# Kernel optimization log

Hardware: AMD Instinct MI355X
Metric: run time of the kernel (lower is better)

The kernel has to match this reference:

```python
import jax, jax.numpy as jnp
import numpy as np

IN_FEATURES = 4096
OUT_FEATURES = 4096  # % 16 == 0, so pad_out = 0
BATCH, SEQ = 4, 2048


def setup_inputs() -> dict:
    key = jax.random.key(0)
    k_x, k_w, k_b = jax.random.split(key, 3)
    # int8 activations and weights (W8A8)
    x = jax.random.randint(k_x, (BATCH, SEQ, IN_FEATURES), -128, 128, dtype=jnp.int32).astype(jnp.int8)
    # weight stored as (in_features, out_features), matching qlinear.weight layout
    weight = jax.random.randint(k_w, (IN_FEATURES, OUT_FEATURES), -128, 128, dtype=jnp.int32).astype(jnp.int8)
    # a: scalar input scale; b: per-output-channel dequant/requant scale
    a = jnp.full((1, 1), 0.0123, dtype=jnp.float32)
    b = jax.random.uniform(k_b, (1, OUT_FEATURES), dtype=jnp.float32, minval=0.001, maxval=0.02)
    return {"x": x, "weight": weight, "a": a, "b": b}


def reference(x, weight, a, b):
    # x: [B, S, K] int8; weight: [K, N] int8; a: [1,1] f32; b: [1,N] f32
    x_shape = x.shape
    x2d = x.reshape(-1, x_shape[-1])
    acc = jnp.matmul(x2d, weight, preferred_element_type=jnp.int32)
    # fused dequant (scalar a) + per-channel requant (b), round-to-nearest, saturate to int8
    y_f = acc.astype(jnp.float32) * a * b  # [T, N]
    y = jnp.clip(jnp.round(y_f), -128.0, 127.0).astype(jnp.int8)
    return y.reshape(*x_shape[:-1], -1)
```

## Files before the change

kernel.cpp:

```cpp
#include <hip/hip_runtime.h>
#include <stdint.h>

#define M_DIM 8192
#define N_DIM 4096
#define K_DIM 4096
#define BM 128
#define BN 128
#define BK 64

typedef int v4i __attribute__((ext_vector_type(4)));
typedef unsigned u32;

__device__ __forceinline__ void gll16(const void* g, void* l) {
  __builtin_amdgcn_global_load_lds(
      (const __attribute__((address_space(1))) void*)g,
      (__attribute__((address_space(3))) void*)l, 16, 0, 0);
}

__device__ __forceinline__ u32 pack4(const int4 v) {
  return (v.x & 0xffu) | ((v.y & 0xffu) << 8) | ((v.z & 0xffu) << 16) |
         ((u32)(v.w & 0xffu) << 24);
}

__global__ __launch_bounds__(256) void detect_i32(const int* __restrict__ X,
                                                  u32* __restrict__ flag) {
  __shared__ int ok;
  if (threadIdx.x == 0) ok = 1;
  __syncthreads();
  int good = 1;
  for (int i = threadIdx.x; i < 1024; i += 256) {
    const int w = X[i];
    good &= (w == (int)(int8_t)(w & 0xff));
  }
  if (!good) atomicAnd(&ok, 0);
  __syncthreads();
  if (threadIdx.x == 0) *flag = (u32)ok;
}

__global__ __launch_bounds__(256) void pack_x_ad(const void* __restrict__ Xin,
                                                 u32* __restrict__ out,
                                                 const u32* __restrict__ flag) {
  const bool i32 = (*flag != 0);
  const int base = blockIdx.x * 1024 + threadIdx.x;
  if (i32) {
    const int4* in = (const int4*)Xin;
#pragma unroll
    for (int j = 0; j < 4; ++j) {
      const int idx = base + j * 256;
      out[idx] = pack4(in[idx]);
    }
  } else {
    const u32* in = (const u32*)Xin;
#pragma unroll
    for (int j = 0; j < 4; ++j) {
      const int idx = base + j * 256;
      out[idx] = in[idx];
    }
  }
}

__global__ __launch_bounds__(256) void packT_w_ad(const void* __restrict__ Wv,
                                                  int8_t* __restrict__ WT,
                                                  const u32* __restrict__ flag) {
  __shared__ u32 lds[64 * 21];
  const bool i32 = (*flag != 0);
  const int tid = threadIdx.x;
  const int tk = blockIdx.x & 63;
  const int tn = blockIdx.x >> 6;
  const int k0 = tk * 64, n0 = tn * 64;

#pragma unroll
  for (int j = 0; j < 4; ++j) {
    const int id = j * 256 + tid;
    const int k = id >> 4, c = id & 15;
    u32 word;
    if (i32) {
      const int4 v =
          *(const int4*)((const int*)Wv + (size_t)(k0 + k) * N_DIM + n0 + c * 4);
      word = pack4(v);
    } else {
      word = *(const u32*)((const int8_t*)Wv + (size_t)(k0 + k) * N_DIM + n0 +
                           c * 4);
    }
    lds[k * 21 + c] = word;
  }
  __syncthreads();
  const int kd = tid & 15, nq = tid >> 4;
  const u32 d0 = lds[(kd * 4 + 0) * 21 + nq];
  const u32 d1 = lds[(kd * 4 + 1) * 21 + nq];
  const u32 d2 = lds[(kd * 4 + 2) * 21 + nq];
  const u32 d3 = lds[(kd * 4 + 3) * 21 + nq];
  u32* outp = (u32*)WT;
#pragma unroll
  for (int i = 0; i < 4; ++i) {
    const u32 e = ((d0 >> (8 * i)) & 0xffu) | (((d1 >> (8 * i)) & 0xffu) << 8) |
                  (((d2 >> (8 * i)) & 0xffu) << 16) |
                  (((d3 >> (8 * i)) & 0xffu) << 24);
    const int n = n0 + nq * 4 + i;
    outp[(size_t)n * (K_DIM / 4) + (k0 / 4) + kd] = e;
  }
}

__device__ __forceinline__ void epilogue(const v4i acc[4][4], float a,
                                         const float* __restrict__ bScale,
                                         int* __restrict__ Y, int bm, int bn,
                                         int wm, int wn, int quad, int l16) {
  const int nBase = bn * BN + wn * 64 + l16;
  float bs[4];
#pragma unroll
  for (int ni = 0; ni < 4; ++ni) bs[ni] = bScale[nBase + ni * 16];
#pragma unroll
  for (int mi = 0; mi < 4; ++mi) {
    const int m0 = bm * BM + wm * 64 + mi * 16 + quad * 4;
#pragma unroll
    for (int r = 0; r < 4; ++r) {
      int* row = Y + (size_t)(m0 + r) * N_DIM + nBase;
#pragma unroll
      for (int ni = 0; ni < 4; ++ni) {
        float v = ((float)acc[mi][ni][r] * a) * bs[ni];
        v = rintf(v);
        v = fminf(fmaxf(v, -128.f), 127.f);
        row[ni * 16] = (int)v;
      }
    }
  }
}

__global__ __launch_bounds__(512, 2) void gemm_256(
    const int8_t* __restrict__ X, const int8_t* __restrict__ WT,
    const float* __restrict__ aScale, const float* __restrict__ bScale,
    int* __restrict__ Y) {
  __shared__ __align__(16) int8_t lds[131072];
  const int tid = threadIdx.x;
  const int lane = tid & 63;
  const int wave = tid >> 6;
  const int quad = lane >> 4, l16 = lane & 15;
  const int wm = wave >> 2, wn = wave & 3;

  const int swz = (blockIdx.x & 7) * 64 + (blockIdx.x >> 3);
  const int bn = swz & 15, bm = swz >> 4;

  const int clog = (((tid & 3) ^ ((tid >> 3) & 3)) << 4);
  const int pc = quad ^ ((l16 >> 1) & 3);

  const int8_t* xa = X + (size_t)(bm * 256 + (tid >> 2)) * K_DIM + clog;
  const int8_t* xb = WT + (size_t)(bn * 256 + (tid >> 2)) * K_DIM + clog;
  int8_t* ldsA = lds + tid * 16;
  int8_t* ldsB = lds + 65536 + tid * 16;
  const int8_t* aBase = lds + (wm * 128 + l16) * 64 + pc * 16;
  const int8_t* bBase = lds + 65536 + (wn * 64 + l16) * 64 + pc * 16;

  v4i acc[8][4] = {};

  gll16(xa, ldsA);
  gll16(xa + (size_t)128 * K_DIM, ldsA + 8192);
  gll16(xb, ldsB);
  gll16(xb + (size_t)128 * K_DIM, ldsB + 8192);
  gll16(xa + 64, ldsA + 16384);
  gll16(xa + (size_t)128 * K_DIM + 64, ldsA + 16384 + 8192);
  gll16(xb + 64, ldsB + 16384);
  gll16(xb + (size_t)128 * K_DIM + 64, ldsB + 16384 + 8192);
  asm volatile("s_waitcnt vmcnt(4)" ::: "memory");
  __builtin_amdgcn_s_barrier();

  for (int g = 0; g < 64; ++g) {
    const int soff = (g & 3) << 14;
    const int poff = ((g + 2) & 3) << 14;
    const bool pre = (g + 2) < 64;
    v4i af[4], bf[4];
#pragma unroll
    for (int i = 0; i < 4; ++i)
      af[i] = *(const v4i*)(aBase + soff + i * 1024);
#pragma unroll
    for (int i = 0; i < 4; ++i)
      bf[i] = *(const v4i*)(bBase + soff + i * 1024);
    if (pre) {
      const int8_t* s = xa + (size_t)(g + 2) * 64;
      gll16(s, ldsA + poff);
      gll16(s + (size_t)128 * K_DIM, ldsA + poff + 8192);
    }
    __builtin_amdgcn_s_barrier();
    asm volatile("s_waitcnt lgkmcnt(0)" ::: "memory");
    __builtin_amdgcn_sched_barrier(0);
    __builtin_amdgcn_s_setprio(1);
#pragma unroll
    for (int mi = 0; mi < 4; ++mi)
#pragma unroll
      for (int ni = 0; ni < 4; ++ni)
        acc[mi][ni] = __builtin_amdgcn_mfma_i32_16x16x64_i8(
            af[mi], bf[ni], acc[mi][ni], 0, 0, 0);
    __builtin_amdgcn_s_setprio(0);
    __builtin_amdgcn_s_barrier();

#pragma unroll
    for (int i = 0; i < 4; ++i)
      af[i] = *(const v4i*)(aBase + soff + 4096 + i * 1024);
    if (pre) {
      const int8_t* s = xb + (size_t)(g + 2) * 64;
      gll16(s, ldsB + poff);
      gll16(s + (size_t)128 * K_DIM, ldsB + poff + 8192);
    }
    __builtin_amdgcn_s_barrier();
    asm volatile("s_waitcnt lgkmcnt(0)" ::: "memory");
    __builtin_amdgcn_sched_barrier(0);
    __builtin_amdgcn_s_setprio(1);
#pragma unroll
    for (int mi = 0; mi < 4; ++mi)
#pragma unroll
      for (int ni = 0; ni < 4; ++ni)
        acc[4 + mi][ni] = __builtin_amdgcn_mfma_i32_16x16x64_i8(
            af[mi], bf[ni], acc[4 + mi][ni], 0, 0, 0);
    __builtin_amdgcn_s_setprio(0);
    if (g <= 61)
      asm volatile("s_waitcnt vmcnt(4)" ::: "memory");
    else
      asm volatile("s_waitcnt vmcnt(0)" ::: "memory");
    __builtin_amdgcn_s_barrier();
  }

  const float a = aScale[0];
  const int nBase = bn * 256 + wn * 64 + l16;
  float bs[4];
#pragma unroll
  for (int ni = 0; ni < 4; ++ni) bs[ni] = bScale[nBase + ni * 16];
#pragma unroll
  for (int mi = 0; mi < 8; ++mi) {
    const int m0 = bm * 256 + wm * 128 + mi * 16 + quad * 4;
#pragma unroll
    for (int r = 0; r < 4; ++r) {
      int* row = Y + (size_t)(m0 + r) * N_DIM + nBase;
#pragma unroll
      for (int ni = 0; ni < 4; ++ni) {
        float v = ((float)acc[mi][ni][r] * a) * bs[ni];
        v = rintf(v);
        v = fminf(fmaxf(v, -128.f), 127.f);
        row[ni * 16] = (int)v;
      }
    }
  }
}

__global__ __launch_bounds__(256) void gemm_inA(
    const void* __restrict__ Xv, const int8_t* __restrict__ WT,
    const float* __restrict__ aScale, const float* __restrict__ bScale,
    int* __restrict__ Y, const u32* __restrict__ flag) {
  __shared__ __align__(16) int8_t As[BM * BK];
  __shared__ __align__(16) int8_t Bs[BN * BK];
  const bool i32 = (*flag != 0);
  const int tid = threadIdx.x;
  const int lane = tid & 63, wave = tid >> 6;
  const int quad = lane >> 4, l16 = lane & 15;
  const int wm = wave & 1, wn = wave >> 1;
  const int bn = blockIdx.x & 31;
  const int bm = blockIdx.x >> 5;

  const int r0 = tid >> 2;
  const int c0 = (tid & 3) * 16;
  const int8_t* Bg0 = WT + (size_t)(bn * BN + r0) * K_DIM + c0;
  const int8_t* Bg1 = Bg0 + (size_t)64 * K_DIM;
  int8_t* Al0 = As + tid * 16;
  int8_t* Al1 = Al0 + 4096;
  int8_t* Bl0 = Bs + tid * 16;
  int8_t* Bl1 = Bl0 + 4096;

  v4i acc[4][4] = {};
  const int8_t* aLds = As + (wm * 64 + l16) * BK + quad * 16;
  const int8_t* bLds = Bs + (wn * 64 + l16) * BK + quad * 16;

  if (i32) {
    const int* Xg0 = (const int*)Xv + (size_t)(bm * BM + r0) * K_DIM + c0;
    const int* Xg1 = Xg0 + (size_t)64 * K_DIM;
    for (int k0 = 0; k0 < K_DIM; k0 += BK) {
      gll16(Bg0 + k0, Bl0);
      gll16(Bg1 + k0, Bl1);
      const int4* p0 = (const int4*)(Xg0 + k0);
      const int4* p1 = (const int4*)(Xg1 + k0);
      uint4 w0, w1;
      w0.x = pack4(p0[0]); w0.y = pack4(p0[1]);
      w0.z = pack4(p0[2]); w0.w = pack4(p0[3]);
      w1.x = pack4(p1[0]); w1.y = pack4(p1[1]);
      w1.z = pack4(p1[2]); w1.w = pack4(p1[3]);
      *(uint4*)Al0 = w0;
      *(uint4*)Al1 = w1;
      __syncthreads();
      v4i af[4], bf[4];
#pragma unroll
      for (int i = 0; i < 4; ++i) af[i] = *(const v4i*)(aLds + i * 16 * BK);
#pragma unroll
      for (int i = 0; i < 4; ++i) bf[i] = *(const v4i*)(bLds + i * 16 * BK);
#pragma unroll
      for (int mi = 0; mi < 4; ++mi)
#pragma unroll
        for (int ni = 0; ni < 4; ++ni)
          acc[mi][ni] = __builtin_amdgcn_mfma_i32_16x16x64_i8(
              af[mi], bf[ni], acc[mi][ni], 0, 0, 0);
      __syncthreads();
    }
  } else {
    const int8_t* Ag0 = (const int8_t*)Xv + (size_t)(bm * BM + r0) * K_DIM + c0;
    const int8_t* Ag1 = Ag0 + (size_t)64 * K_DIM;
    for (int k0 = 0; k0 < K_DIM; k0 += BK) {
      gll16(Ag0 + k0, Al0);
      gll16(Ag1 + k0, Al1);
      gll16(Bg0 + k0, Bl0);
      gll16(Bg1 + k0, Bl1);
      __syncthreads();
      v4i af[4], bf[4];
#pragma unroll
      for (int i = 0; i < 4; ++i) af[i] = *(const v4i*)(aLds + i * 16 * BK);
#pragma unroll
      for (int i = 0; i < 4; ++i) bf[i] = *(const v4i*)(bLds + i * 16 * BK);
#pragma unroll
      for (int mi = 0; mi < 4; ++mi)
#pragma unroll
        for (int ni = 0; ni < 4; ++ni)
          acc[mi][ni] = __builtin_amdgcn_mfma_i32_16x16x64_i8(
              af[mi], bf[ni], acc[mi][ni], 0, 0, 0);
      __syncthreads();
    }
  }
  epilogue(acc, aScale[0], bScale, Y, bm, bn, wm, wn, quad, l16);
}

extern "C" void kernel_launch(void* const* d_in, const int* in_sizes, int n_in,
                              void* d_out, int out_size, void* d_ws,
                              size_t ws_size, hipStream_t stream) {
  const void* Xv = d_in[0];
  const void* Wv = d_in[1];
  const float* a = (const float*)d_in[2];
  const float* b = (const float*)d_in[3];
  int* Y = (int*)d_out;

  const size_t xB = (size_t)M_DIM * K_DIM;
  const size_t wB = (size_t)N_DIM * K_DIM;

  if (ws_size >= xB + wB + 64) {
    int8_t* Xp = (int8_t*)d_ws;
    int8_t* WT = (int8_t*)d_ws + xB;
    u32* flag = (u32*)((int8_t*)d_ws + xB + wB);
    detect_i32<<<1, 256, 0, stream>>>((const int*)Xv, flag);
    pack_x_ad<<<(M_DIM * K_DIM / 4) / 1024, 256, 0, stream>>>(Xv, (u32*)Xp,
                                                              flag);
    packT_w_ad<<<(K_DIM / 64) * (N_DIM / 64), 256, 0, stream>>>(Wv, WT, flag);
    gemm_256<<<(M_DIM / 256) * (N_DIM / 256), 512, 0, stream>>>(Xp, WT, a, b,
                                                                Y);
  } else if (ws_size >= wB + 64) {
    int8_t* WT = (int8_t*)d_ws;
    u32* flag = (u32*)((int8_t*)d_ws + wB);
    detect_i32<<<1, 256, 0, stream>>>((const int*)Xv, flag);
    packT_w_ad<<<(K_DIM / 64) * (N_DIM / 64), 256, 0, stream>>>(Wv, WT, flag);
    gemm_inA<<<(M_DIM / BM) * (N_DIM / BN), 256, 0, stream>>>(Xv, WT, a, b, Y,
                                                              flag);
  } else {
    int8_t* WT = (int8_t*)d_ws;
    u32* flag = (u32*)((int8_t*)d_ws + (ws_size >= wB + 4 ? wB : 0));
    detect_i32<<<1, 256, 0, stream>>>((const int*)Xv, flag);
    packT_w_ad<<<(K_DIM / 64) * (N_DIM / 64), 256, 0, stream>>>(Wv, WT, flag);
    gemm_inA<<<(M_DIM / BM) * (N_DIM / BN), 256, 0, stream>>>(Xv, WT, a, b, Y,
                                                              flag);
  }
}
```

Baseline: 408.0 us.

## Switch GEMM to 32x32x32 int8 MFMA, deepen prefetch, inline dtype detection

The main 256x256 GEMM now uses 32x32x32 int8 MFMA tiles with v16i accumulators instead of 16x16x64 tiles. This halves the B-fragment register count per wave, and the epilogue is rewritten for the 32x32 output layout. The global-to-LDS prefetch goes from two stages ahead to three stages ahead, using all four LDS slots, with the vmcnt waits adjusted to match. The separate detect_i32 kernel launch is dropped on the main path: each pack block now re-checks the input header itself, which trades a launch and a dependency for redundant small reads per block.

```diff
diff --git a/kernel.cpp b/kernel.cpp
--- a/kernel.cpp
+++ b/kernel.cpp
@@ -9,6 +9,7 @@
 #define BK 64
 
 typedef int v4i __attribute__((ext_vector_type(4)));
+typedef int v16i __attribute__((ext_vector_type(16)));
 typedef unsigned u32;
 
 __device__ __forceinline__ void gll16(const void* g, void* l) {
@@ -22,25 +23,31 @@
          ((u32)(v.w & 0xffu) << 24);
 }
 
+__device__ __forceinline__ bool hdr_is_i32(const int* __restrict__ X, int tid,
+                                           int* ok) {
+  if (tid == 0) *ok = 1;
+  __syncthreads();
+  int good = 1;
+  for (int i = tid; i < 1024; i += 256) {
+    const int w = X[i];
+    good &= (w == (int)(int8_t)(w & 0xff));
+  }
+  if (!good) atomicAnd(ok, 0);
+  __syncthreads();
+  return *ok != 0;
+}
+
 __global__ __launch_bounds__(256) void detect_i32(const int* __restrict__ X,
                                                   u32* __restrict__ flag) {
   __shared__ int ok;
-  if (threadIdx.x == 0) ok = 1;
-  __syncthreads();
-  int good = 1;
-  for (int i = threadIdx.x; i < 1024; i += 256) {
-    const int w = X[i];
-    good &= (w == (int)(int8_t)(w & 0xff));
-  }
-  if (!good) atomicAnd(&ok, 0);
-  __syncthreads();
-  if (threadIdx.x == 0) *flag = (u32)ok;
-}
-
-__global__ __launch_bounds__(256) void pack_x_ad(const void* __restrict__ Xin,
-                                                 u32* __restrict__ out,
-                                                 const u32* __restrict__ flag) {
-  const bool i32 = (*flag != 0);
+  const bool i32 = hdr_is_i32(X, threadIdx.x, &ok);
+  if (threadIdx.x == 0) *flag = i32 ? 1u : 0u;
+}
+
+__global__ __launch_bounds__(256) void pack_x_f(const void* __restrict__ Xin,
+                                                u32* __restrict__ out) {
+  __shared__ int ok;
+  const bool i32 = hdr_is_i32((const int*)Xin, threadIdx.x, &ok);
   const int base = blockIdx.x * 1024 + threadIdx.x;
   if (i32) {
     const int4* in = (const int4*)Xin;
@@ -59,12 +66,13 @@
   }
 }
 
-__global__ __launch_bounds__(256) void packT_w_ad(const void* __restrict__ Wv,
-                                                  int8_t* __restrict__ WT,
-                                                  const u32* __restrict__ flag) {
+__global__ __launch_bounds__(256) void packT_w_f(const void* __restrict__ Wv,
+                                                 int8_t* __restrict__ WT,
+                                                 const int* __restrict__ Xhdr) {
   __shared__ u32 lds[64 * 21];
-  const bool i32 = (*flag != 0);
+  __shared__ int ok;
   const int tid = threadIdx.x;
+  const bool i32 = hdr_is_i32(Xhdr, tid, &ok);
   const int tk = blockIdx.x & 63;
   const int tn = blockIdx.x >> 6;
   const int k0 = tk * 64, n0 = tn * 64;
@@ -134,48 +142,51 @@
   const int tid = threadIdx.x;
   const int lane = tid & 63;
   const int wave = tid >> 6;
-  const int quad = lane >> 4, l16 = lane & 15;
+  const int l31 = lane & 31, h = lane >> 5;
   const int wm = wave >> 2, wn = wave & 3;
 
-  const int swz = (blockIdx.x & 7) * 64 + (blockIdx.x >> 3);
-  const int bn = swz & 15, bm = swz >> 4;
+  const int swzb = (blockIdx.x & 7) * 64 + (blockIdx.x >> 3);
+  const int bn = swzb & 15, bm = swzb >> 4;
 
   const int clog = (((tid & 3) ^ ((tid >> 3) & 3)) << 4);
-  const int pc = quad ^ ((l16 >> 1) & 3);
+  const int sw = (l31 >> 1) & 3;
+  const int pc0 = (h ^ sw) << 4;
+  const int pc1 = pc0 ^ 32;
 
   const int8_t* xa = X + (size_t)(bm * 256 + (tid >> 2)) * K_DIM + clog;
   const int8_t* xb = WT + (size_t)(bn * 256 + (tid >> 2)) * K_DIM + clog;
   int8_t* ldsA = lds + tid * 16;
   int8_t* ldsB = lds + 65536 + tid * 16;
-  const int8_t* aBase = lds + (wm * 128 + l16) * 64 + pc * 16;
-  const int8_t* bBase = lds + 65536 + (wn * 64 + l16) * 64 + pc * 16;
-
-  v4i acc[8][4] = {};
-
-  gll16(xa, ldsA);
-  gll16(xa + (size_t)128 * K_DIM, ldsA + 8192);
-  gll16(xb, ldsB);
-  gll16(xb + (size_t)128 * K_DIM, ldsB + 8192);
-  gll16(xa + 64, ldsA + 16384);
-  gll16(xa + (size_t)128 * K_DIM + 64, ldsA + 16384 + 8192);
-  gll16(xb + 64, ldsB + 16384);
-  gll16(xb + (size_t)128 * K_DIM + 64, ldsB + 16384 + 8192);
-  asm volatile("s_waitcnt vmcnt(4)" ::: "memory");
+  const int8_t* aB0 = lds + (wm * 128 + l31) * 64 + pc0;
+  const int8_t* aB1 = lds + (wm * 128 + l31) * 64 + pc1;
+  const int8_t* bB0 = lds + 65536 + (wn * 64 + l31) * 64 + pc0;
+  const int8_t* bB1 = lds + 65536 + (wn * 64 + l31) * 64 + pc1;
+
+  v16i acc[4][2] = {};
+
+#pragma unroll
+  for (int t = 0; t < 3; ++t) {
+    gll16(xa + t * 64, ldsA + t * 16384);
+    gll16(xa + (size_t)128 * K_DIM + t * 64, ldsA + t * 16384 + 8192);
+    gll16(xb + t * 64, ldsB + t * 16384);
+    gll16(xb + (size_t)128 * K_DIM + t * 64, ldsB + t * 16384 + 8192);
+  }
+  asm volatile("s_waitcnt vmcnt(8)" ::: "memory");
   __builtin_amdgcn_s_barrier();
 
   for (int g = 0; g < 64; ++g) {
     const int soff = (g & 3) << 14;
-    const int poff = ((g + 2) & 3) << 14;
-    const bool pre = (g + 2) < 64;
-    v4i af[4], bf[4];
-#pragma unroll
-    for (int i = 0; i < 4; ++i)
-      af[i] = *(const v4i*)(aBase + soff + i * 1024);
-#pragma unroll
-    for (int i = 0; i < 4; ++i)
-      bf[i] = *(const v4i*)(bBase + soff + i * 1024);
+    const int poff = ((g + 3) & 3) << 14;
+    const bool pre = g <= 60;
+    v4i af[4], bf[2];
+#pragma unroll
+    for (int mi = 0; mi < 4; ++mi)
+      af[mi] = *(const v4i*)(aB0 + soff + mi * 2048);
+#pragma unroll
+    for (int ni = 0; ni < 2; ++ni)
+      bf[ni] = *(const v4i*)(bB0 + soff + ni * 2048);
     if (pre) {
-      const int8_t* s = xa + (size_t)(g + 2) * 64;
+      const int8_t* s = xa + (size_t)(g + 3) * 64;
       gll16(s, ldsA + poff);
       gll16(s + (size_t)128 * K_DIM, ldsA + poff + 8192);
     }
@@ -186,17 +197,20 @@
 #pragma unroll
     for (int mi = 0; mi < 4; ++mi)
 #pragma unroll
-      for (int ni = 0; ni < 4; ++ni)
-        acc[mi][ni] = __builtin_amdgcn_mfma_i32_16x16x64_i8(
+      for (int ni = 0; ni < 2; ++ni)
+        acc[mi][ni] = __builtin_amdgcn_mfma_i32_32x32x32_i8(
             af[mi], bf[ni], acc[mi][ni], 0, 0, 0);
     __builtin_amdgcn_s_setprio(0);
     __builtin_amdgcn_s_barrier();
 
 #pragma unroll
-    for (int i = 0; i < 4; ++i)
-      af[i] = *(const v4i*)(aBase + soff + 4096 + i * 1024);
+    for (int mi = 0; mi < 4; ++mi)
+      af[mi] = *(const v4i*)(aB1 + soff + mi * 2048);
+#pragma unroll
+    for (int ni = 0; ni < 2; ++ni)
+      bf[ni] = *(const v4i*)(bB1 + soff + ni * 2048);
     if (pre) {
-      const int8_t* s = xb + (size_t)(g + 2) * 64;
+      const int8_t* s = xb + (size_t)(g + 3) * 64;
       gll16(s, ldsB + poff);
       gll16(s + (size_t)128 * K_DIM, ldsB + poff + 8192);
     }
@@ -207,11 +221,13 @@
 #pragma unroll
     for (int mi = 0; mi < 4; ++mi)
 #pragma unroll
-      for (int ni = 0; ni < 4; ++ni)
-        acc[4 + mi][ni] = __builtin_amdgcn_mfma_i32_16x16x64_i8(
-            af[mi], bf[ni], acc[4 + mi][ni], 0, 0, 0);
+      for (int ni = 0; ni < 2; ++ni)
+        acc[mi][ni] = __builtin_amdgcn_mfma_i32_32x32x32_i8(
+            af[mi], bf[ni], acc[mi][ni], 0, 0, 0);
     __builtin_amdgcn_s_setprio(0);
-    if (g <= 61)
+    if (g < 61)
+      asm volatile("s_waitcnt vmcnt(8)" ::: "memory");
+    else if (g == 61)
       asm volatile("s_waitcnt vmcnt(4)" ::: "memory");
     else
       asm volatile("s_waitcnt vmcnt(0)" ::: "memory");
@@ -219,22 +235,23 @@
   }
 
   const float a = aScale[0];
-  const int nBase = bn * 256 + wn * 64 + l16;
-  float bs[4];
-#pragma unroll
-  for (int ni = 0; ni < 4; ++ni) bs[ni] = bScale[nBase + ni * 16];
-#pragma unroll
-  for (int mi = 0; mi < 8; ++mi) {
-    const int m0 = bm * 256 + wm * 128 + mi * 16 + quad * 4;
-#pragma unroll
-    for (int r = 0; r < 4; ++r) {
-      int* row = Y + (size_t)(m0 + r) * N_DIM + nBase;
-#pragma unroll
-      for (int ni = 0; ni < 4; ++ni) {
-        float v = ((float)acc[mi][ni][r] * a) * bs[ni];
+  const int nB = bn * 256 + wn * 64 + l31;
+  const float bs0 = bScale[nB];
+  const float bs1 = bScale[nB + 32];
+#pragma unroll
+  for (int mi = 0; mi < 4; ++mi) {
+#pragma unroll
+    for (int ni = 0; ni < 2; ++ni) {
+      const float bsv = ni ? bs1 : bs0;
+      const int nCol = nB + ni * 32;
+#pragma unroll
+      for (int r = 0; r < 16; ++r) {
+        const int row =
+            bm * 256 + wm * 128 + mi * 32 + (r & 3) + 8 * (r >> 2) + 4 * h;
+        float v = ((float)acc[mi][ni][r] * a) * bsv;
         v = rintf(v);
         v = fminf(fmaxf(v, -128.f), 127.f);
-        row[ni * 16] = (int)v;
+        Y[(size_t)row * N_DIM + nCol] = (int)v;
       }
     }
   }
@@ -337,25 +354,25 @@
   if (ws_size >= xB + wB + 64) {
     int8_t* Xp = (int8_t*)d_ws;
     int8_t* WT = (int8_t*)d_ws + xB;
-    u32* flag = (u32*)((int8_t*)d_ws + xB + wB);
-    detect_i32<<<1, 256, 0, stream>>>((const int*)Xv, flag);
-    pack_x_ad<<<(M_DIM * K_DIM / 4) / 1024, 256, 0, stream>>>(Xv, (u32*)Xp,
-                                                              flag);
-    packT_w_ad<<<(K_DIM / 64) * (N_DIM / 64), 256, 0, stream>>>(Wv, WT, flag);
+    pack_x_f<<<(M_DIM * K_DIM / 4) / 1024, 256, 0, stream>>>(Xv, (u32*)Xp);
+    packT_w_f<<<(K_DIM / 64) * (N_DIM / 64), 256, 0, stream>>>(Wv, WT,
+                                                               (const int*)Xv);
     gemm_256<<<(M_DIM / 256) * (N_DIM / 256), 512, 0, stream>>>(Xp, WT, a, b,
                                                                 Y);
   } else if (ws_size >= wB + 64) {
     int8_t* WT = (int8_t*)d_ws;
     u32* flag = (u32*)((int8_t*)d_ws + wB);
     detect_i32<<<1, 256, 0, stream>>>((const int*)Xv, flag);
-    packT_w_ad<<<(K_DIM / 64) * (N_DIM / 64), 256, 0, stream>>>(Wv, WT, flag);
+    packT_w_f<<<(K_DIM / 64) * (N_DIM / 64), 256, 0, stream>>>(Wv, WT,
+                                                               (const int*)Xv);
     gemm_inA<<<(M_DIM / BM) * (N_DIM / BN), 256, 0, stream>>>(Xv, WT, a, b, Y,
                                                               flag);
   } else {
     int8_t* WT = (int8_t*)d_ws;
     u32* flag = (u32*)((int8_t*)d_ws + (ws_size >= wB + 4 ? wB : 0));
     detect_i32<<<1, 256, 0, stream>>>((const int*)Xv, flag);
-    packT_w_ad<<<(K_DIM / 64) * (N_DIM / 64), 256, 0, stream>>>(Wv, WT, flag);
+    packT_w_f<<<(K_DIM / 64) * (N_DIM / 64), 256, 0, stream>>>(Wv, WT,
+                                                               (const int*)Xv);
     gemm_inA<<<(M_DIM / BM) * (N_DIM / BN), 256, 0, stream>>>(Xv, WT, a, b, Y,
                                                               flag);
   }
```

After: 438.2 us. 1.07x slower.
